# Kernel tuning notes

Measured on AMD Instinct MI355X. Metric: run time of the kernel, lower is better.

Reference implementation:

```python
import jax, jax.numpy as jnp
import numpy as np

B, Qn, Kn, QD, KVD, FFN, H = 8, 1024, 2048, 512, 256, 2048, 8


def _layer_norm(x, g, b, eps=1e-5):
    m = jnp.mean(x, axis=-1, keepdims=True)
    v = jnp.mean((x - m) ** 2, axis=-1, keepdims=True)
    return (x - m) * jax.lax.rsqrt(v + eps) * g + b


def _mha(q, k, v, key_padding_mask, num_heads):
    # q,k: [B,S,D], v: [B,K,Dv]; reshape to per-head, scale by sqrt(key head dim)
    b, qn, d = q.shape
    kn = k.shape[1]
    dh = d // num_heads
    q = q.reshape(b, qn, num_heads, dh)
    k = k.reshape(b, kn, num_heads, dh)
    v = v.reshape(b, kn, num_heads, -1)
    attn = jnp.einsum('bqhd,bkhd->bhqk', q, k) / jnp.asarray(np.sqrt(dh), q.dtype)
    attn = jnp.where(key_padding_mask[:, None, None, :], -jnp.inf, attn)
    attn = jax.nn.softmax(attn, axis=-1)
    out = jnp.einsum('bhqk,bkhd->bqhd', attn, v)  # [B,Q,H,dv]
    return out.reshape(b, qn, -1)


def setup_inputs() -> dict:
    key = jax.random.key(0)
    ks = jax.random.split(key, 32)
    s = 0.02
    inp = {
        'queries_data': jax.random.normal(ks[0], (B, Qn, QD), jnp.float32),
        'queries_mask': jnp.zeros((B, Qn), bool),
        'box_pos': jax.random.normal(ks[1], (B, Qn, 4 * KVD), jnp.float32),
        'center_pos': jax.random.normal(ks[2], (B, Qn, 2 * KVD), jnp.float32),
        'kv_data': jax.random.normal(ks[3], (B, Kn, KVD), jnp.float32),
        'kv_mask': jnp.zeros((B, Kn), bool),
        'kv_pos': jax.random.normal(ks[4], (B, Kn, KVD), jnp.float32),
        # params ([in,out] convention)
        'sa_qkv_w': jax.random.normal(ks[5], (QD, 3 * QD), jnp.float32) * s,
        'sa_qkv_b': jnp.zeros((3 * QD,), jnp.float32),
        'sa_pos_w': jax.random.normal(ks[6], (4 * KVD, 2 * QD), jnp.float32) * s,
        'sa_pos_b': jnp.zeros((2 * QD,), jnp.float32),
        'sa_ln_g': jnp.ones((QD,), jnp.float32),
        'sa_ln_b': jnp.zeros((QD,), jnp.float32),
        'ca_q_w': jax.random.normal(ks[7], (QD, QD), jnp.float32) * s,
        'ca_q_b': jnp.zeros((QD,), jnp.float32),
        'ca_kv_w': jax.random.normal(ks[8], (KVD, 2 * QD), jnp.float32) * s,
        'ca_kv_b': jnp.zeros((2 * QD,), jnp.float32),
        'ca_qpos_w': jax.random.normal(ks[9], (2 * KVD, QD), jnp.float32) * s,
        'ca_qpos_b': jnp.zeros((QD,), jnp.float32),
        'ca_kpos_w': jax.random.normal(ks[10], (KVD, QD), jnp.float32) * s,
        'ca_kpos_b': jnp.zeros((QD,), jnp.float32),
        'ca_ln_g': jnp.ones((QD,), jnp.float32),
        'ca_ln_b': jnp.zeros((QD,), jnp.float32),
        'ffn_w1': jax.random.normal(ks[11], (QD, FFN), jnp.float32) * s,
        'ffn_b1': jnp.zeros((FFN,), jnp.float32),
        'ffn_w2': jax.random.normal(ks[12], (FFN, QD), jnp.float32) * s,
        'ffn_b2': jnp.zeros((QD,), jnp.float32),
        'ffn_ln_g': jnp.ones((QD,), jnp.float32),
        'ffn_ln_b': jnp.zeros((QD,), jnp.float32),
    }
    return inp


def reference(queries_data, queries_mask, box_pos, center_pos, kv_data, kv_mask, kv_pos,
              sa_qkv_w, sa_qkv_b, sa_pos_w, sa_pos_b, sa_ln_g, sa_ln_b,
              ca_q_w, ca_q_b, ca_kv_w, ca_kv_b, ca_qpos_w, ca_qpos_b,
              ca_kpos_w, ca_kpos_b, ca_ln_g, ca_ln_b,
              ffn_w1, ffn_b1, ffn_w2, ffn_b2, ffn_ln_g, ffn_ln_b):
    # ---- self-attention (pos added to q,k) ----
    qkv = queries_data @ sa_qkv_w + sa_qkv_b
    q, k, v = jnp.split(qkv, 3, axis=-1)
    q_pos, k_pos = jnp.split(box_pos @ sa_pos_w + sa_pos_b, 2, axis=-1)
    sa_out = _mha(q + q_pos, k + k_pos, v, queries_mask, H)
    sa_out = _layer_norm(queries_data + sa_out, sa_ln_g, sa_ln_b)
    # ---- cross-attention (pos concatenated per head) ----
    q = sa_out @ ca_q_w + ca_q_b
    k, v = jnp.split(kv_data @ ca_kv_w + ca_kv_b, 2, axis=-1)
    q_pos = center_pos @ ca_qpos_w + ca_qpos_b
    k_pos = kv_pos @ ca_kpos_w + ca_kpos_b
    dh = QD // H
    q = jnp.concatenate([q.reshape(B, Qn, H, dh), q_pos.reshape(B, Qn, H, dh)], axis=-1).reshape(B, Qn, -1)
    k = jnp.concatenate([k.reshape(B, Kn, H, dh), k_pos.reshape(B, Kn, H, dh)], axis=-1).reshape(B, Kn, -1)
    ca_out = _mha(q, k, v, kv_mask, H)
    ca_out = _layer_norm(sa_out + ca_out, ca_ln_g, ca_ln_b)
    # ---- FFN ----
    f = jax.nn.relu(ca_out @ ffn_w1 + ffn_b1) @ ffn_w2 + ffn_b2
    return _layer_norm(ca_out + f, ffn_ln_g, ffn_ln_b)
```

## Files before the change

kernel.cpp:

```cpp
#include <hip/hip_runtime.h>

typedef __attribute__((ext_vector_type(4))) float f32x4;
typedef __attribute__((ext_vector_type(8))) short bf16x8;
typedef __attribute__((ext_vector_type(4))) unsigned int u32x4;

static __device__ __forceinline__ short f2bf(float f){
    unsigned int u = __builtin_bit_cast(unsigned int, f);
    unsigned int r = (u + 0x7fffu + ((u >> 16) & 1u)) >> 16;
    return (short)r;
}
static __device__ __forceinline__ void gload_lds16(const void* g, void* l){
    __builtin_amdgcn_global_load_lds((const __attribute__((address_space(1))) void*)g,
                                     (__attribute__((address_space(3))) void*)l, 16, 0, 0);
}
static __device__ __forceinline__ float exp2fast(float x){
    float r; asm("v_exp_f32 %0, %1" : "=v"(r) : "v"(x)); return r;
}
static __device__ __forceinline__ unsigned int packbf(float lo, float hi){
#if __has_builtin(__builtin_amdgcn_perm)
    return __builtin_amdgcn_perm(__builtin_bit_cast(unsigned int, hi),
                                 __builtin_bit_cast(unsigned int, lo), 0x07060302u);
#else
    return (__builtin_bit_cast(unsigned int, hi) & 0xffff0000u) |
           (__builtin_bit_cast(unsigned int, lo) >> 16);
#endif
}
static __device__ __forceinline__ void prio_hi(){
#if defined(__HIP_DEVICE_COMPILE__)
    __builtin_amdgcn_s_setprio(1);
#endif
}
static __device__ __forceinline__ void prio_lo(){
#if defined(__HIP_DEVICE_COMPILE__)
    __builtin_amdgcn_s_setprio(0);
#endif
}

static __device__ __forceinline__ void transcast_body(const float* __restrict__ w,
                                                      short* __restrict__ wT,
                                                      int K, int N, int bx, int by, int t){
    int n = bx * 256 + t;
    int k0 = by * 8;
    bf16x8 o;
#pragma unroll
    for (int j = 0; j < 8; j++) o[j] = f2bf(w[(long)(k0 + j) * N + n]);
    *(bf16x8*)(wT + (long)n * K + k0) = o;
}
__global__ __launch_bounds__(256) void prep_weights(
    const float* __restrict__ queries, const float* __restrict__ box,
    const float* __restrict__ ctr, const float* __restrict__ kvd, const float* __restrict__ kvp,
    const unsigned char* __restrict__ qmask, const unsigned char* __restrict__ kmask,
    const float* __restrict__ b_qkv, const float* __restrict__ b_pos,
    short* __restrict__ Xcat, short* __restrict__ ctr_bf,
    short* __restrict__ kvd_bf, short* __restrict__ kvp_bf,
    float* __restrict__ mb_sa, float* __restrict__ mb_ca, float* __restrict__ bcomb,
    const float* __restrict__ w_qkv, const float* __restrict__ w_pos,
    const float* __restrict__ w_caq, const float* __restrict__ w_cakv,
    const float* __restrict__ w_caqp, const float* __restrict__ w_cakp,
    const float* __restrict__ w_f1, const float* __restrict__ w_f2,
    short* __restrict__ wTm_qk, short* __restrict__ wTv,
    short* __restrict__ wT_caq, short* __restrict__ wT_cakv,
    short* __restrict__ wT_caqp, short* __restrict__ wT_cakp,
    short* __restrict__ wT_f1, short* __restrict__ wT_f2)
{
    int bb = blockIdx.x, t = threadIdx.x;
    if (bb < 12288){
        const float* src; short* dst; long i; long stride; int logRow; int colOff;
        if (bb < 2048){ src = queries; dst = Xcat; i = ((long)bb * 256 + t) * 8; logRow = 9;  stride = 1536; colOff = 0; }
        else if (bb < 6144){ src = box; dst = Xcat; i = ((long)(bb - 2048) * 256 + t) * 8; logRow = 10; stride = 1536; colOff = 512; }
        else if (bb < 8192){ src = ctr; dst = ctr_bf; i = ((long)(bb - 6144) * 256 + t) * 8; logRow = 0; stride = 0; colOff = 0; }
        else if (bb < 10240){ src = kvd; dst = kvd_bf; i = ((long)(bb - 8192) * 256 + t) * 8; logRow = 0; stride = 0; colOff = 0; }
        else { src = kvp; dst = kvp_bf; i = ((long)(bb - 10240) * 256 + t) * 8; logRow = 0; stride = 0; colOff = 0; }
        f32x4 a = *(const f32x4*)(src + i);
        f32x4 b = *(const f32x4*)(src + i + 4);
        bf16x8 o;
#pragma unroll
        for (int j = 0; j < 4; j++){ o[j] = f2bf(a[j]); o[4 + j] = f2bf(b[j]); }
        long oi = logRow ? ((i >> logRow) * stride + colOff + (i & ((1L << logRow) - 1))) : i;
        *(bf16x8*)(dst + oi) = o;
        return;
    }
    if (bb < 12320){ int i = (bb - 12288) * 256 + t; mb_sa[i] = qmask[i] ? -1e30f : 0.f; return; }
    if (bb < 12384){ int i = (bb - 12320) * 256 + t; mb_ca[i] = kmask[i] ? -1e30f : 0.f; return; }
    if (bb < 12388){ int i = (bb - 12384) * 256 + t; if (i < 1024) bcomb[i] = b_qkv[i] + b_pos[i]; return; }
    int wb = bb - 12388;
    if (wb < 768){
        int by = wb / 4, bx = wb % 4;
        int n = bx * 256 + t;
        int k0 = by * 8;
        bf16x8 o;
#pragma unroll
        for (int j = 0; j < 8; j++){
            int kk = k0 + j;
            float v = (kk < 512) ? w_qkv[(long)kk * 1536 + n] : w_pos[(long)(kk - 512) * 1024 + n];
            o[j] = f2bf(v);
        }
        *(bf16x8*)(wTm_qk + (long)n * 1536 + k0) = o;
    }
    else if (wb < 896){
        int lb = wb - 768;
        int by = lb / 2, bx = lb % 2;
        int n = bx * 256 + t;
        int k0 = by * 8;
        bf16x8 o;
#pragma unroll
        for (int j = 0; j < 8; j++) o[j] = f2bf(w_qkv[(long)(k0 + j) * 1536 + 1024 + n]);
        *(bf16x8*)(wTv + (long)n * 512 + k0) = o;
    }
    else if (wb < 1024){ int lb = wb - 896;  transcast_body(w_caq,  wT_caq,  512, 512,  lb % 2, lb / 2, t); }
    else if (wb < 1152){ int lb = wb - 1024; transcast_body(w_cakv, wT_cakv, 256, 1024, lb % 4, lb / 4, t); }
    else if (wb < 1280){ int lb = wb - 1152; transcast_body(w_caqp, wT_caqp, 512, 512,  lb % 2, lb / 2, t); }
    else if (wb < 1344){ int lb = wb - 1280; transcast_body(w_cakp, wT_cakp, 256, 512,  lb % 2, lb / 2, t); }
    else if (wb < 1856){ int lb = wb - 1344; transcast_body(w_f1,   wT_f1,   512, 2048, lb % 8, lb / 8, t); }
    else               { int lb = wb - 1856; transcast_body(w_f2,   wT_f2,   2048, 512, lb % 2, lb / 2, t); }
}

template<int BN>
__global__ __launch_bounds__((BN == 64) ? 128 : 256, 3) void gemm_bf16(
    const short* __restrict__ A, long lda, const short* __restrict__ Bt,
    const float* __restrict__ bias,
    short* __restrict__ Cbf, float* __restrict__ Cf, int M, int N, int K, int flags,
    short* __restrict__ Vt, int vtColBase, int snShift, int vtSN)
{
    constexpr int BLOCK = (BN == 64) ? 128 : 256;
    constexpr int NW = BLOCK / 64;
    constexpr int BUF = (128 + BN) * 32;
    constexpr int EST = BN + 4;
    constexpr int SB = 2 * BUF * 2;
    constexpr int EB = 32 * EST * 4;
    constexpr int SMB = SB > EB ? SB : EB;
    __shared__ __attribute__((aligned(16))) char smem[SMB];
    float* lC = (float*)smem;
    int t = threadIdx.x, w = t >> 6, l = t & 63;
    int cl = l & 15, g = l >> 4;
    int nbx = gridDim.x;
    int flat = blockIdx.y * nbx + blockIdx.x;
    int q8 = (nbx * gridDim.y) >> 3;
    int swz = (flat & 7) * q8 + (flat >> 3);
    long r0 = (long)(swz / nbx) * 128, c0 = (long)(swz % nbx) * BN;
    int wr = (NW == 2) ? w : (w >> 1);
    int wc = (NW == 2) ? 0 : (w & 1);
    f32x4 acc[4][4];
#pragma unroll
    for (int mi = 0; mi < 4; mi++)
#pragma unroll
        for (int ni = 0; ni < 4; ni++) acc[mi][ni] = f32x4{0.f, 0.f, 0.f, 0.f};

    auto stage = [&](int d, int k0){
        char* lA = smem + (size_t)d * BUF * 2;
        char* lB = lA + 128 * 32 * 2;
#pragma unroll
        for (int i = 0; i < 512 / BLOCK; i++){
            int s = i * BLOCK + t;
            int row = s >> 2, blk = s & 3;
            int sb = blk ^ (row & 3);
            gload_lds16(A + (r0 + row) * lda + k0 + sb * 8, lA + i * (BLOCK * 16) + w * 1024);
        }
#pragma unroll
        for (int i = 0; i < BN * 4 / BLOCK; i++){
            int s = i * BLOCK + t;
            int row = s >> 2, blk = s & 3;
            int sb = blk ^ (row & 3);
            gload_lds16(Bt + (c0 + row) * (long)K + k0 + sb * 8, lB + i * (BLOCK * 16) + w * 1024);
        }
    };

    stage(0, 0);
    __syncthreads();
    int NK = K / 32;
    for (int kt = 0; kt < NK; kt++){
        int cur = kt & 1;
        if (kt + 1 < NK) stage(cur ^ 1, (kt + 1) * 32);
        const short* lA = (const short*)(smem + (size_t)cur * BUF * 2);
        const short* lB = lA + 128 * 32;
        bf16x8 af[4], bfr[4];
#pragma unroll
        for (int mi = 0; mi < 4; mi++){
            int row = wr * 64 + mi * 16 + cl;
            af[mi] = *(const bf16x8*)(lA + row * 32 + (g ^ (row & 3)) * 8);
        }
#pragma unroll
        for (int ni = 0; ni < 4; ni++){
            int row = wc * 64 + ni * 16 + cl;
            bfr[ni] = *(const bf16x8*)(lB + row * 32 + (g ^ (row & 3)) * 8);
        }
        prio_hi();
#pragma unroll
        for (int mi = 0; mi < 4; mi++)
#pragma unroll
            for (int ni = 0; ni < 4; ni++)
                acc[mi][ni] = __builtin_amdgcn_mfma_f32_16x16x32_bf16(af[mi], bfr[ni], acc[mi][ni], 0, 0, 0);
        prio_lo();
        __syncthreads();
    }

    bool vtBlock = (flags & 4) && (c0 >= vtColBase);
#pragma unroll
    for (int mi = 0; mi < 4; mi++){
        __syncthreads();
#pragma unroll
        for (int ni = 0; ni < 4; ni++)
#pragma unroll
            for (int rr = 0; rr < 4; rr++)
                lC[(wr * 16 + g * 4 + rr) * EST + wc * 64 + ni * 16 + cl] = acc[mi][ni][rr];
        __syncthreads();
        if (vtBlock){
#pragma unroll
            for (int c2 = 0; c2 < BN * 4 / BLOCK; c2++){
                int task = t + BLOCK * c2;
                int col = task & (BN - 1);
                int wrg = (task / BN) & 1;
                int ch = task / (BN * 2);
                float bv = bias[c0 + col];
                long qg0 = r0 + wrg * 64 + mi * 16 + ch * 8;
                bf16x8 ob;
#pragma unroll
                for (int j = 0; j < 8; j++)
                    ob[j] = f2bf(lC[(wrg * 16 + ch * 8 + j) * EST + col] + bv);
                long dvg = c0 - vtColBase + col;
                long h = dvg >> 6, dvv = dvg & 63;
                long b = qg0 >> snShift;
                long loc = qg0 & ((1L << snShift) - 1);
                *(bf16x8*)(Vt + ((b * 8 + h) * 64 + dvv) * (long)vtSN + loc) = ob;
            }
        } else {
            constexpr int CPR = BN / 8;
#pragma unroll
            for (int c2 = 0; c2 < 32 * CPR / BLOCK; c2++){
                int chunk = t + BLOCK * c2;
                int row = chunk / CPR;
                int coloff = (chunk % CPR) * 8;
                long grow = r0 + (row >> 4) * 64 + mi * 16 + (row & 15);
                long gcol = c0 + coloff;
                f32x4 bv0 = *(const f32x4*)(bias + gcol);
                f32x4 bv1 = *(const f32x4*)(bias + gcol + 4);
                float v[8];
#pragma unroll
                for (int j = 0; j < 8; j++){
                    float x = lC[row * EST + coloff + j] + (j < 4 ? bv0[j] : bv1[j - 4]);
                    if (flags & 1) x = fmaxf(x, 0.f);
                    v[j] = x;
                }
                if (Cf){
                    *(f32x4*)(Cf + grow * N + gcol) = f32x4{v[0], v[1], v[2], v[3]};
                    *(f32x4*)(Cf + grow * N + gcol + 4) = f32x4{v[4], v[5], v[6], v[7]};
                } else {
                    bf16x8 ob;
#pragma unroll
                    for (int j = 0; j < 8; j++) ob[j] = f2bf(v[j]);
                    long idx;
                    if (flags & 2){
                        long part = gcol >> 9;
                        long cc = gcol & 511;
                        long b = grow >> 10, qn = grow & 1023;
                        long h = cc >> 6, d = cc & 63;
                        idx = ((part * 64 + b * 8 + h) * 1024 + qn) * 64 + d;
                    } else if (flags & 4){
                        idx = grow * (long)vtColBase + gcol;
                    } else {
                        idx = grow * N + gcol;
                    }
                    *(bf16x8*)(Cbf + idx) = ob;
                }
            }
        }
    }
}

__global__ __launch_bounds__(256) void ln_fuse(const float* __restrict__ a, const float* __restrict__ b,
                                               const float* __restrict__ g, const float* __restrict__ be,
                                               float* __restrict__ outf, short* __restrict__ outb){
    int w = threadIdx.x >> 6, l = threadIdx.x & 63;
    long row = (long)blockIdx.x * 4 + w;
    long base = row * 512 + l * 8;
    f32x4 a0 = *(const f32x4*)(a + base);
    f32x4 a1 = *(const f32x4*)(a + base + 4);
    f32x4 b0 = *(const f32x4*)(b + base);
    f32x4 b1 = *(const f32x4*)(b + base + 4);
    float x[8]; float s = 0.f, s2 = 0.f;
#pragma unroll
    for (int j = 0; j < 4; j++){ x[j] = a0[j] + b0[j]; x[4 + j] = a1[j] + b1[j]; }
#pragma unroll
    for (int j = 0; j < 8; j++){ s += x[j]; s2 += x[j] * x[j]; }
#pragma unroll
    for (int o = 1; o < 64; o <<= 1){ s += __shfl_xor(s, o); s2 += __shfl_xor(s2, o); }
    float mean = s * (1.f / 512.f);
    float rstd = rsqrtf(s2 * (1.f / 512.f) - mean * mean + 1e-5f);
    int c = l * 8;
    f32x4 y0, y1; bf16x8 ob;
#pragma unroll
    for (int j = 0; j < 4; j++){
        float y = (x[j] - mean) * rstd * g[c + j] + be[c + j];
        y0[j] = y; ob[j] = f2bf(y);
    }
#pragma unroll
    for (int j = 0; j < 4; j++){
        float y = (x[4 + j] - mean) * rstd * g[c + 4 + j] + be[c + 4 + j];
        y1[j] = y; ob[4 + j] = f2bf(y);
    }
    *(f32x4*)(outf + base) = y0;
    *(f32x4*)(outf + base + 4) = y1;
    if (outb) *(bf16x8*)(outb + base) = ob;
}

template<int DH, int KN, bool CAT>
__global__ __launch_bounds__(256, 2) void attn_kernel(
    const short* __restrict__ Q1, const short* __restrict__ Q2,
    const short* __restrict__ K1, const short* __restrict__ K2,
    const short* __restrict__ Vt,
    const float* __restrict__ mbias, float* __restrict__ out, float scale2)
{
    constexpr int KT = 64, DV = 64, Qn = 1024, H = 8;
    constexpr int NF = DH / 32;
    constexpr int BPR = DH / 8;
    constexpr int KITER = KT * BPR / 256;
    constexpr int NT = KN / KT;
    __shared__ __attribute__((aligned(16))) short lK[2][KT * DH];
    __shared__ __attribute__((aligned(16))) short lV[2][DV * KT];
    int t = threadIdx.x, w = t >> 6, l = t & 63;
    int cl = l & 15, g = l >> 4;
    int bid = blockIdx.x;
    int bh = (bid & 7) * 8 + (bid >> 6);
    int qb = (bid >> 3) & 7;
    int b = bh >> 3, h = bh & 7;
    int q0 = qb * 128 + w * 32;

    bf16x8 qf[2][NF];
#pragma unroll
    for (int qq = 0; qq < 2; qq++)
#pragma unroll
        for (int f = 0; f < NF; f++){
            if constexpr (CAT){
                const short* src = (f < NF / 2) ? Q1 : Q2;
                qf[qq][f] = *(const bf16x8*)(src + ((long)b * Qn + q0 + qq * 16 + cl) * 512 + h * 64
                                             + (f & (NF / 2 - 1)) * 32 + 8 * g);
            } else {
                qf[qq][f] = *(const bf16x8*)(Q1 + ((long)bh * Qn + q0 + qq * 16 + cl) * DH + f * 32 + 8 * g);
            }
        }

    const short* kp[KITER];
    long kstep[KITER];
#pragma unroll
    for (int i = 0; i < KITER; i++){
        int s_ = i * 256 + t;
        int srow_ = s_ / BPR, blk = s_ % BPR;
        int s32 = srow_ & 31;
        int key = (srow_ & 32) + 8 * ((s32 >> 2) & 3) + 4 * (s32 >> 4) + (s32 & 3);
        int sb = blk ^ (srow_ & 7);
        if constexpr (CAT){
            if (sb < 8){ kp[i] = K1 + ((long)b * KN + key) * 512 + h * 64 + sb * 8; kstep[i] = (long)KT * 512; }
            else       { kp[i] = K2 + ((long)b * KN + key) * 512 + h * 64 + (sb - 8) * 8; kstep[i] = (long)KT * 512; }
        } else {
            kp[i] = K1 + ((long)bh * KN + key) * DH + sb * 8; kstep[i] = (long)KT * DH;
        }
    }
    const short* vp[2];
#pragma unroll
    for (int i = 0; i < 2; i++){
        int s_ = i * 256 + t;
        int srow_ = s_ >> 3, blk = s_ & 7;
        int sb = blk ^ (srow_ & 7);
        vp[i] = Vt + ((long)bh * DV + srow_) * KN + sb * 8;
    }

    auto stage = [&](int d){
#pragma unroll
        for (int i = 0; i < KITER; i++){
            gload_lds16(kp[i], (char*)(&lK[d][0]) + i * 4096 + w * 1024);
            kp[i] += kstep[i];
        }
#pragma unroll
        for (int i = 0; i < 2; i++){
            gload_lds16(vp[i], (char*)(&lV[d][0]) + i * 4096 + w * 1024);
            vp[i] += KT;
        }
    };

    f32x4 st[2][4];
    auto do_qk = [&](int d){
        prio_hi();
#pragma unroll
        for (int o = 0; o < 4; o++){
            int srow_ = o * 16 + cl;
            bf16x8 kf[NF];
#pragma unroll
            for (int f = 0; f < NF; f++){
                int sb = (4 * f + g) ^ (srow_ & 7);
                kf[f] = *(const bf16x8*)(&lK[d][0] + srow_ * DH + sb * 8);
            }
#pragma unroll
            for (int qq = 0; qq < 2; qq++){
                f32x4 acc = f32x4{0.f, 0.f, 0.f, 0.f};
#pragma unroll
                for (int f = 0; f < NF; f++)
                    acc = __builtin_amdgcn_mfma_f32_16x16x32_bf16(kf[f], qf[qq][f], acc, 0, 0, 0);
                st[qq][o] = acc;
            }
        }
        prio_lo();
    };

    const float* mrow = mbias + (long)b * KN;
    bf16x8 vones;
    {
        u32x4 ou; ou[0] = ou[1] = ou[2] = ou[3] = 0x3F803F80u;
        vones = __builtin_bit_cast(bf16x8, ou);
    }
    f32x4 lacc[2];
    f32x4 oacc[2][4];
#pragma unroll
    for (int qq = 0; qq < 2; qq++){
        lacc[qq] = f32x4{0.f, 0.f, 0.f, 0.f};
#pragma unroll
        for (int d = 0; d < 4; d++) oacc[qq][d] = f32x4{0.f, 0.f, 0.f, 0.f};
    }

    f32x4 mb[4];
#pragma unroll
    for (int o = 0; o < 4; o++)
        mb[o] = *(const f32x4*)(mrow + (o >> 1) * 32 + 8 * g + 4 * (o & 1));

    stage(0);
    __syncthreads();
    do_qk(0);

    for (int tt = 0; tt < NT; tt++){
        int cur = tt & 1;
        if (tt + 1 < NT) stage(cur ^ 1);

        bf16x8 pa[2][2];
#pragma unroll
        for (int qq = 0; qq < 2; qq++){
#pragma unroll
            for (int kb = 0; kb < 2; kb++){
                float pA[4], pB[4];
#pragma unroll
                for (int rr = 0; rr < 4; rr++){
                    pA[rr] = exp2fast(fmaf(st[qq][2 * kb][rr], scale2, mb[2 * kb][rr]));
                    pB[rr] = exp2fast(fmaf(st[qq][2 * kb + 1][rr], scale2, mb[2 * kb + 1][rr]));
                }
                u32x4 pk;
                pk[0] = packbf(pA[0], pA[1]);
                pk[1] = packbf(pA[2], pA[3]);
                pk[2] = packbf(pB[0], pB[1]);
                pk[3] = packbf(pB[2], pB[3]);
                pa[qq][kb] = __builtin_bit_cast(bf16x8, pk);
            }
        }
        if (tt + 1 < NT){
#pragma unroll
            for (int o = 0; o < 4; o++)
                mb[o] = *(const f32x4*)(mrow + (tt + 1) * KT + (o >> 1) * 32 + 8 * g + 4 * (o & 1));
        }
        prio_hi();
#pragma unroll
        for (int qq = 0; qq < 2; qq++){
            lacc[qq] = __builtin_amdgcn_mfma_f32_16x16x32_bf16(pa[qq][0], vones, lacc[qq], 0, 0, 0);
            lacc[qq] = __builtin_amdgcn_mfma_f32_16x16x32_bf16(pa[qq][1], vones, lacc[qq], 0, 0, 0);
        }
#pragma unroll
        for (int dvc = 0; dvc < 4; dvc++){
            int vrow = dvc * 16 + cl;
            bf16x8 vf[2];
#pragma unroll
            for (int kb = 0; kb < 2; kb++){
                int sb = (4 * kb + g) ^ (vrow & 7);
                vf[kb] = *(const bf16x8*)(&lV[cur][0] + vrow * KT + sb * 8);
            }
#pragma unroll
            for (int qq = 0; qq < 2; qq++){
                f32x4 o = oacc[qq][dvc];
                o = __builtin_amdgcn_mfma_f32_16x16x32_bf16(pa[qq][0], vf[0], o, 0, 0, 0);
                o = __builtin_amdgcn_mfma_f32_16x16x32_bf16(pa[qq][1], vf[1], o, 0, 0, 0);
                oacc[qq][dvc] = o;
            }
        }
        prio_lo();
        __syncthreads();
        if (tt + 1 < NT) do_qk(cur ^ 1);
    }

#pragma unroll
    for (int qq = 0; qq < 2; qq++){
        float linv[4];
#pragma unroll
        for (int rr = 0; rr < 4; rr++) linv[rr] = 1.f / lacc[qq][rr];
#pragma unroll
        for (int dvc = 0; dvc < 4; dvc++)
#pragma unroll
            for (int rr = 0; rr < 4; rr++){
                int q = q0 + qq * 16 + 4 * g + rr;
                out[(((long)b * Qn + q) * H + h) * DV + dvc * 16 + cl] = oacc[qq][dvc][rr] * linv[rr];
            }
    }
}

extern "C" void kernel_launch(void* const* d_in, const int* in_sizes, int n_in,
                              void* d_out, int out_size, void* d_ws, size_t ws_size,
                              hipStream_t stream)
{
    (void)in_sizes; (void)n_in; (void)out_size; (void)ws_size;
    const int Qn = 1024, Kn = 2048;
    const long MQ = 8L * Qn;
    const long MK = 8L * Kn;

    const float* queries = (const float*)d_in[0];
    const unsigned char* qmask = (const unsigned char*)d_in[1];
    const float* box  = (const float*)d_in[2];
    const float* ctr  = (const float*)d_in[3];
    const float* kvd  = (const float*)d_in[4];
    const unsigned char* kmask = (const unsigned char*)d_in[5];
    const float* kvp  = (const float*)d_in[6];
    const float* w_qkv = (const float*)d_in[7];  const float* b_qkv = (const float*)d_in[8];
    const float* w_pos = (const float*)d_in[9];  const float* b_pos = (const float*)d_in[10];
    const float* g_sa  = (const float*)d_in[11]; const float* be_sa = (const float*)d_in[12];
    const float* w_caq = (const float*)d_in[13]; const float* b_caq = (const float*)d_in[14];
    const float* w_cakv = (const float*)d_in[15]; const float* b_cakv = (const float*)d_in[16];
    const float* w_caqp = (const float*)d_in[17]; const float* b_caqp = (const float*)d_in[18];
    const float* w_cakp = (const float*)d_in[19]; const float* b_cakp = (const float*)d_in[20];
    const float* g_ca  = (const float*)d_in[21]; const float* be_ca = (const float*)d_in[22];
    const float* w_f1  = (const float*)d_in[23]; const float* b_f1 = (const float*)d_in[24];
    const float* w_f2  = (const float*)d_in[25]; const float* b_f2 = (const float*)d_in[26];
    const float* g_f   = (const float*)d_in[27]; const float* be_f = (const float*)d_in[28];

    char* ws = (char*)d_ws;
    size_t off = 0;
    auto alloc = [&](size_t bytes) -> char* {
        char* p = ws + off;
        off += (bytes + 255) & ~(size_t)255;
        return p;
    };
    short* wTm_qk  = (short*)alloc(1024L * 1536 * 2);
    short* wTv     = (short*)alloc(512L * 512 * 2);
    short* wT_caq  = (short*)alloc(512L * 512 * 2);
    short* wT_cakv = (short*)alloc(1024L * 256 * 2);
    short* wT_caqp = (short*)alloc(512L * 512 * 2);
    short* wT_cakp = (short*)alloc(512L * 256 * 2);
    short* wT_f1   = (short*)alloc(2048L * 512 * 2);
    short* wT_f2   = (short*)alloc(512L * 2048 * 2);
    float* bcomb   = (float*)alloc(1024L * 4);
    short* ctr_bf  = (short*)alloc(MQ * 512 * 2);
    short* kvd_bf  = (short*)alloc(MK * 256 * 2);
    short* kvp_bf  = (short*)alloc(MK * 256 * 2);
    short* saln_bf = (short*)alloc(MQ * 512 * 2);
    short* caln_bf = (short*)alloc(MQ * 512 * 2);
    float* sa_ln_f = (float*)alloc(MQ * 512 * 4);
    float* ca_ln_f = (float*)alloc(MQ * 512 * 4);
    float* att_f   = (float*)alloc(MQ * 512 * 4);
    float* f_out   = (float*)alloc(MQ * 512 * 4);
    short* VtSA    = (short*)alloc(64L * 64 * 1024 * 2);
    short* VtCA    = (short*)alloc(64L * 64 * 2048 * 2);
    float* mb_sa   = (float*)alloc(MQ * 4);
    float* mb_ca   = (float*)alloc(MK * 4);
    char* zone1 = alloc(MK * 1024 * 2);
    char* zone2 = alloc(MQ * 2048 * 2);
    char* zone3 = alloc(MK * 512 * 2);
    char* zone4 = alloc(MQ * 512 * 2);
    char* zone5 = alloc(MQ * 512 * 2);

    auto gemm128 = [&](const short* A, long lda, const short* Bt, const float* bias,
                       short* Cbf, float* Cf, int M, int N, int K, int flags,
                       short* Vt, int vtColBase, int snShift, int vtSN){
        gemm_bf16<128><<<dim3(N / 128, M / 128), dim3(256), 0, stream>>>(
            A, lda, Bt, bias, Cbf, Cf, M, N, K, flags, Vt, vtColBase, snShift, vtSN);
    };
    auto gemm64 = [&](const short* A, long lda, const short* Bt, const float* bias,
                      short* Cbf, float* Cf, int M, int N, int K, int flags,
                      short* Vt, int vtColBase, int snShift, int vtSN){
        gemm_bf16<64><<<dim3(N / 64, M / 128), dim3(128), 0, stream>>>(
            A, lda, Bt, bias, Cbf, Cf, M, N, K, flags, Vt, vtColBase, snShift, vtSN);
    };

    short* Xcat = (short*)zone1;
    prep_weights<<<dim3(14756), dim3(256), 0, stream>>>(
        queries, box, ctr, kvd, kvp, qmask, kmask, b_qkv, b_pos,
        Xcat, ctr_bf, kvd_bf, kvp_bf, mb_sa, mb_ca, bcomb,
        w_qkv, w_pos, w_caq, w_cakv, w_caqp, w_cakp, w_f1, w_f2,
        wTm_qk, wTv, wT_caq, wT_cakv, wT_caqp, wT_cakp, wT_f1, wT_f2);

    short* QKVa = (short*)zone2;
    short* Qa  = QKVa;
    short* Ka  = QKVa + 64L * 1024 * 64;
    gemm128(Xcat, 1536, wTm_qk, bcomb, QKVa, nullptr, (int)MQ, 1024, 1536, 2, nullptr, 0, 0, 0);
    gemm64(Xcat, 1536, wTv, b_qkv + 1024, nullptr, nullptr, (int)MQ, 512, 512, 4, VtSA, 0, 10, 1024);

    attn_kernel<64, 1024, false><<<dim3(512), dim3(256), 0, stream>>>(
        Qa, nullptr, Ka, nullptr, VtSA, mb_sa, att_f, 0.125f * 1.44269504f);

    ln_fuse<<<dim3((unsigned)(MQ / 4)), dim3(256), 0, stream>>>(queries, att_f, g_sa, be_sa, sa_ln_f, saln_bf);

    short* caq_bf  = (short*)zone4;
    short* caqp_bf = (short*)zone5;
    short* caK     = (short*)zone1;
    short* cakp_bf = (short*)zone3;
    gemm64(saln_bf, 512, wT_caq, b_caq, caq_bf, nullptr, (int)MQ, 512, 512, 0, nullptr, 0, 0, 0);
    gemm64(ctr_bf, 512, wT_caqp, b_caqp, caqp_bf, nullptr, (int)MQ, 512, 512, 0, nullptr, 0, 0, 0);
    gemm128(kvd_bf, 256, wT_cakv, b_cakv, caK, nullptr, (int)MK, 1024, 256, 4, VtCA, 512, 11, 2048);
    gemm64(kvp_bf, 256, wT_cakp, b_cakp, cakp_bf, nullptr, (int)MK, 512, 256, 0, nullptr, 0, 0, 0);

    attn_kernel<128, 2048, true><<<dim3(512), dim3(256), 0, stream>>>(
        caq_bf, caqp_bf, caK, cakp_bf, VtCA, mb_ca, att_f, 0.08838834764831845f * 1.44269504f);

    ln_fuse<<<dim3((unsigned)(MQ / 4)), dim3(256), 0, stream>>>(sa_ln_f, att_f, g_ca, be_ca, ca_ln_f, caln_bf);

    short* mid_bf = (short*)zone2;
    gemm128(caln_bf, 512, wT_f1, b_f1, mid_bf, nullptr, (int)MQ, 2048, 512, 1, nullptr, 0, 0, 0);
    gemm64(mid_bf, 2048, wT_f2, b_f2, nullptr, f_out, (int)MQ, 512, 2048, 0, nullptr, 0, 0, 0);

    ln_fuse<<<dim3((unsigned)(MQ / 4)), dim3(256), 0, stream>>>(ca_ln_f, f_out, g_f, be_f, (float*)d_out, (short*)nullptr);
}
```

Measured before the change: 320.9 us.

## Batch independent GEMMs into grouped multi-problem launches with uniform 128x64 tiles

Replaces the two templated GEMM variants with a single 128x64-tile kernel that takes a descriptor table of up to four GEMM problems and maps each block to a problem by block-index ranges. The self-attention QKV and V GEMMs are merged into one launch, and the four cross-attention projection GEMMs into another. The goal is to cut launch count and fill the GPU better with small independent GEMMs. In exchange, the large-N GEMMs (QK and FFN1) lose their 128x128 tiles, which lowers data reuse per block and adds a per-block descriptor lookup.

```diff
diff --git a/kernel.cpp b/kernel.cpp
--- a/kernel.cpp
+++ b/kernel.cpp
@@ -115,31 +115,43 @@
     else               { int lb = wb - 1856; transcast_body(w_f2,   wT_f2,   2048, 512, lb % 2, lb / 2, t); }
 }
 
-template<int BN>
-__global__ __launch_bounds__((BN == 64) ? 128 : 256, 3) void gemm_bf16(
-    const short* __restrict__ A, long lda, const short* __restrict__ Bt,
-    const float* __restrict__ bias,
-    short* __restrict__ Cbf, float* __restrict__ Cf, int M, int N, int K, int flags,
-    short* __restrict__ Vt, int vtColBase, int snShift, int vtSN)
+struct GD {
+    const short* A; const short* Bt; const float* bias;
+    short* Cbf; float* Cf; short* Vt;
+    long lda;
+    int N, K, flags, vtColBase, snShift, vtSN, blkStart, nbx, nblk;
+};
+struct GD4 { GD g[4]; int n; };
+
+__global__ __launch_bounds__(128, 3) void gemm_multi(GD4 dd)
 {
-    constexpr int BLOCK = (BN == 64) ? 128 : 256;
-    constexpr int NW = BLOCK / 64;
+    constexpr int BN = 64, BLOCK = 128;
     constexpr int BUF = (128 + BN) * 32;
     constexpr int EST = BN + 4;
-    constexpr int SB = 2 * BUF * 2;
-    constexpr int EB = 32 * EST * 4;
-    constexpr int SMB = SB > EB ? SB : EB;
-    __shared__ __attribute__((aligned(16))) char smem[SMB];
+    __shared__ __attribute__((aligned(16))) char smem[2 * BUF * 2];
     float* lC = (float*)smem;
+    int bb = blockIdx.x;
+    int si = 0;
+#pragma unroll
+    for (int i = 1; i < 4; i++) if (i < dd.n && bb >= dd.g[i].blkStart) si = i;
+    const short* A = dd.g[si].A;
+    const short* Bt = dd.g[si].Bt;
+    const float* bias = dd.g[si].bias;
+    short* Cbf = dd.g[si].Cbf;
+    float* Cf = dd.g[si].Cf;
+    short* Vt = dd.g[si].Vt;
+    long lda = dd.g[si].lda;
+    int N = dd.g[si].N, K = dd.g[si].K, flags = dd.g[si].flags;
+    int vtColBase = dd.g[si].vtColBase, snShift = dd.g[si].snShift, vtSN = dd.g[si].vtSN;
+    int nbx = dd.g[si].nbx, nblk = dd.g[si].nblk;
+
     int t = threadIdx.x, w = t >> 6, l = t & 63;
     int cl = l & 15, g = l >> 4;
-    int nbx = gridDim.x;
-    int flat = blockIdx.y * nbx + blockIdx.x;
-    int q8 = (nbx * gridDim.y) >> 3;
+    int flat = bb - dd.g[si].blkStart;
+    int q8 = nblk >> 3;
     int swz = (flat & 7) * q8 + (flat >> 3);
     long r0 = (long)(swz / nbx) * 128, c0 = (long)(swz % nbx) * BN;
-    int wr = (NW == 2) ? w : (w >> 1);
-    int wc = (NW == 2) ? 0 : (w & 1);
+    int wr = w;
     f32x4 acc[4][4];
 #pragma unroll
     for (int mi = 0; mi < 4; mi++)
@@ -150,14 +162,14 @@
         char* lA = smem + (size_t)d * BUF * 2;
         char* lB = lA + 128 * 32 * 2;
 #pragma unroll
-        for (int i = 0; i < 512 / BLOCK; i++){
+        for (int i = 0; i < 4; i++){
             int s = i * BLOCK + t;
             int row = s >> 2, blk = s & 3;
             int sb = blk ^ (row & 3);
             gload_lds16(A + (r0 + row) * lda + k0 + sb * 8, lA + i * (BLOCK * 16) + w * 1024);
         }
 #pragma unroll
-        for (int i = 0; i < BN * 4 / BLOCK; i++){
+        for (int i = 0; i < 2; i++){
             int s = i * BLOCK + t;
             int row = s >> 2, blk = s & 3;
             int sb = blk ^ (row & 3);
@@ -181,7 +193,7 @@
         }
 #pragma unroll
         for (int ni = 0; ni < 4; ni++){
-            int row = wc * 64 + ni * 16 + cl;
+            int row = ni * 16 + cl;
             bfr[ni] = *(const bf16x8*)(lB + row * 32 + (g ^ (row & 3)) * 8);
         }
         prio_hi();
@@ -202,15 +214,15 @@
         for (int ni = 0; ni < 4; ni++)
 #pragma unroll
             for (int rr = 0; rr < 4; rr++)
-                lC[(wr * 16 + g * 4 + rr) * EST + wc * 64 + ni * 16 + cl] = acc[mi][ni][rr];
+                lC[(wr * 16 + g * 4 + rr) * EST + ni * 16 + cl] = acc[mi][ni][rr];
         __syncthreads();
         if (vtBlock){
 #pragma unroll
-            for (int c2 = 0; c2 < BN * 4 / BLOCK; c2++){
+            for (int c2 = 0; c2 < 2; c2++){
                 int task = t + BLOCK * c2;
-                int col = task & (BN - 1);
-                int wrg = (task / BN) & 1;
-                int ch = task / (BN * 2);
+                int col = task & 63;
+                int wrg = (task >> 6) & 1;
+                int ch = task >> 7;
                 float bv = bias[c0 + col];
                 long qg0 = r0 + wrg * 64 + mi * 16 + ch * 8;
                 bf16x8 ob;
@@ -224,12 +236,11 @@
                 *(bf16x8*)(Vt + ((b * 8 + h) * 64 + dvv) * (long)vtSN + loc) = ob;
             }
         } else {
-            constexpr int CPR = BN / 8;
-#pragma unroll
-            for (int c2 = 0; c2 < 32 * CPR / BLOCK; c2++){
+#pragma unroll
+            for (int c2 = 0; c2 < 2; c2++){
                 int chunk = t + BLOCK * c2;
-                int row = chunk / CPR;
-                int coloff = (chunk % CPR) * 8;
+                int row = chunk >> 3;
+                int coloff = (chunk & 7) * 8;
                 long grow = r0 + (row >> 4) * 64 + mi * 16 + (row & 15);
                 long gcol = c0 + coloff;
                 f32x4 bv0 = *(const f32x4*)(bias + gcol);
@@ -559,17 +570,21 @@
     char* zone4 = alloc(MQ * 512 * 2);
     char* zone5 = alloc(MQ * 512 * 2);
 
-    auto gemm128 = [&](const short* A, long lda, const short* Bt, const float* bias,
-                       short* Cbf, float* Cf, int M, int N, int K, int flags,
-                       short* Vt, int vtColBase, int snShift, int vtSN){
-        gemm_bf16<128><<<dim3(N / 128, M / 128), dim3(256), 0, stream>>>(
-            A, lda, Bt, bias, Cbf, Cf, M, N, K, flags, Vt, vtColBase, snShift, vtSN);
+    auto mkgd = [&](const short* A, long lda, const short* Bt, const float* bias,
+                    short* Cbf, float* Cf, int M, int N, int K, int flags,
+                    short* Vt, int vtColBase, int snShift, int vtSN, int blkStart) -> GD {
+        GD d;
+        d.A = A; d.Bt = Bt; d.bias = bias; d.Cbf = Cbf; d.Cf = Cf; d.Vt = Vt;
+        d.lda = lda; d.N = N; d.K = K; d.flags = flags;
+        d.vtColBase = vtColBase; d.snShift = snShift; d.vtSN = vtSN;
+        d.blkStart = blkStart; d.nbx = N / 64; d.nblk = (N / 64) * (M / 128);
+        return d;
     };
-    auto gemm64 = [&](const short* A, long lda, const short* Bt, const float* bias,
-                      short* Cbf, float* Cf, int M, int N, int K, int flags,
-                      short* Vt, int vtColBase, int snShift, int vtSN){
-        gemm_bf16<64><<<dim3(N / 64, M / 128), dim3(128), 0, stream>>>(
-            A, lda, Bt, bias, Cbf, Cf, M, N, K, flags, Vt, vtColBase, snShift, vtSN);
+    auto launch_multi = [&](GD4& dd){
+        int total = 0;
+        for (int i = 0; i < dd.n; i++) total += dd.g[i].nblk;
+        for (int i = dd.n; i < 4; i++){ dd.g[i] = dd.g[0]; dd.g[i].blkStart = 0x7fffffff; }
+        gemm_multi<<<dim3(total), dim3(128), 0, stream>>>(dd);
     };
 
     short* Xcat = (short*)zone1;
@@ -582,8 +597,14 @@
     short* QKVa = (short*)zone2;
     short* Qa  = QKVa;
     short* Ka  = QKVa + 64L * 1024 * 64;
-    gemm128(Xcat, 1536, wTm_qk, bcomb, QKVa, nullptr, (int)MQ, 1024, 1536, 2, nullptr, 0, 0, 0);
-    gemm64(Xcat, 1536, wTv, b_qkv + 1024, nullptr, nullptr, (int)MQ, 512, 512, 4, VtSA, 0, 10, 1024);
+    {
+        GD4 dd; dd.n = 2;
+        dd.g[0] = mkgd(Xcat, 1536, wTm_qk, bcomb, QKVa, nullptr, (int)MQ, 1024, 1536, 2,
+                       nullptr, 0, 0, 0, 0);
+        dd.g[1] = mkgd(Xcat, 1536, wTv, b_qkv + 1024, nullptr, nullptr, (int)MQ, 512, 512, 4,
+                       VtSA, 0, 10, 1024, dd.g[0].nblk);
+        launch_multi(dd);
+    }
 
     attn_kernel<64, 1024, false><<<dim3(512), dim3(256), 0, stream>>>(
         Qa, nullptr, Ka, nullptr, VtSA, mb_sa, att_f, 0.125f * 1.44269504f);
@@ -594,10 +615,19 @@
     short* caqp_bf = (short*)zone5;
     short* caK     = (short*)zone1;
     short* cakp_bf = (short*)zone3;
-    gemm64(saln_bf, 512, wT_caq, b_caq, caq_bf, nullptr, (int)MQ, 512, 512, 0, nullptr, 0, 0, 0);
-    gemm64(ctr_bf, 512, wT_caqp, b_caqp, caqp_bf, nullptr, (int)MQ, 512, 512, 0, nullptr, 0, 0, 0);
-    gemm128(kvd_bf, 256, wT_cakv, b_cakv, caK, nullptr, (int)MK, 1024, 256, 4, VtCA, 512, 11, 2048);
-    gemm64(kvp_bf, 256, wT_cakp, b_cakp, cakp_bf, nullptr, (int)MK, 512, 256, 0, nullptr, 0, 0, 0);
+    {
+        GD4 dd; dd.n = 4;
+        int s0 = 0;
+        dd.g[0] = mkgd(kvd_bf, 256, wT_cakv, b_cakv, caK, nullptr, (int)MK, 1024, 256, 4,
+                       VtCA, 512, 11, 2048, s0);                    s0 += dd.g[0].nblk;
+        dd.g[1] = mkgd(kvp_bf, 256, wT_cakp, b_cakp, cakp_bf, nullptr, (int)MK, 512, 256, 0,
+                       nullptr, 0, 0, 0, s0);                       s0 += dd.g[1].nblk;
+        dd.g[2] = mkgd(saln_bf, 512, wT_caq, b_caq, caq_bf, nullptr, (int)MQ, 512, 512, 0,
+                       nullptr, 0, 0, 0, s0);                       s0 += dd.g[2].nblk;
+        dd.g[3] = mkgd(ctr_bf, 512, wT_caqp, b_caqp, caqp_bf, nullptr, (int)MQ, 512, 512, 0,
+                       nullptr, 0, 0, 0, s0);
+        launch_multi(dd);
+    }
 
     attn_kernel<128, 2048, true><<<dim3(512), dim3(256), 0, stream>>>(
         caq_bf, caqp_bf, caK, cakp_bf, VtCA, mb_ca, att_f, 0.08838834764831845f * 1.44269504f);
@@ -605,8 +635,18 @@
     ln_fuse<<<dim3((unsigned)(MQ / 4)), dim3(256), 0, stream>>>(sa_ln_f, att_f, g_ca, be_ca, ca_ln_f, caln_bf);
 
     short* mid_bf = (short*)zone2;
-    gemm128(caln_bf, 512, wT_f1, b_f1, mid_bf, nullptr, (int)MQ, 2048, 512, 1, nullptr, 0, 0, 0);
-    gemm64(mid_bf, 2048, wT_f2, b_f2, nullptr, f_out, (int)MQ, 512, 2048, 0, nullptr, 0, 0, 0);
+    {
+        GD4 dd; dd.n = 1;
+        dd.g[0] = mkgd(caln_bf, 512, wT_f1, b_f1, mid_bf, nullptr, (int)MQ, 2048, 512, 1,
+                       nullptr, 0, 0, 0, 0);
+        launch_multi(dd);
+    }
+    {
+        GD4 dd; dd.n = 1;
+        dd.g[0] = mkgd(mid_bf, 2048, wT_f2, b_f2, nullptr, f_out, (int)MQ, 512, 2048, 0,
+                       nullptr, 0, 0, 0, 0);
+        launch_multi(dd);
+    }
 
     ln_fuse<<<dim3((unsigned)(MQ / 4)), dim3(256), 0, stream>>>(ca_ln_f, f_out, g_f, be_f, (float*)d_out, (short*)nullptr);
 }
```

After: 317.9 us. Within noise of the previous version (-0.9%).
